# Optimization experiments

Hardware: AMD Instinct MI355X
Metric: run time of the kernel (lower is better)

The kernel has to match this reference:

```python
import jax, jax.numpy as jnp
import numpy as np

HIDDEN = 256
N_PROT = 12288
N_MOL = 6144
N_BATCH = 32


def setup_inputs() -> dict:
    key = jax.random.key(0)
    ks = jax.random.split(key, 10)
    s = 1.0 / np.sqrt(HIDDEN)  # torch Linear default init scale
    inp = {
        "prot_embed": jax.random.normal(ks[0], (N_PROT, HIDDEN), jnp.float32),
        "mol_embed": jax.random.normal(ks[1], (N_MOL, HIDDEN), jnp.float32),
        "prot_batch": jnp.sort(jax.random.randint(ks[2], (N_PROT,), 0, N_BATCH)),
        "mol_batch": jnp.sort(jax.random.randint(ks[3], (N_MOL,), 0, N_BATCH)),
        "Wq": jax.random.uniform(ks[4], (HIDDEN, HIDDEN), jnp.float32, -s, s),
        "bq": jax.random.uniform(ks[5], (HIDDEN,), jnp.float32, -s, s),
        "Wk": jax.random.uniform(ks[6], (HIDDEN, HIDDEN), jnp.float32, -s, s),
        "bk": jax.random.uniform(ks[7], (HIDDEN,), jnp.float32, -s, s),
        "Wv": jax.random.uniform(ks[8], (HIDDEN, HIDDEN), jnp.float32, -s, s),
        "bv": jax.random.uniform(ks[9], (HIDDEN,), jnp.float32, -s, s),
    }
    return inp


def reference(prot_embed, mol_embed, prot_batch, mol_batch, Wq, bq, Wk, bk, Wv, bv):
    # Linear projections (torch nn.Linear: x @ W.T + b)
    Q = prot_embed @ Wq.T + bq            # [N, H]
    K = mol_embed @ Wk.T + bk             # [M, H]
    V = mol_embed @ Wv.T + bv             # [M, H]

    scale = 1.0 / jnp.sqrt(jnp.asarray(Q.shape[-1], Q.dtype))
    scores = (Q @ K.T) * scale            # [N, M]

    # block mask: same-batch pairs only
    mask = prot_batch[:, None] == mol_batch[None, :]   # [N, M] bool
    neg_inf = jnp.asarray(-jnp.inf, scores.dtype)
    scores = jnp.where(mask, scores, neg_inf)

    # stable masked softmax; rows with no valid key -> all zeros
    # (matches torch softmax(-inf row) -> nan -> nan_to_num(0.0))
    row_any = mask.any(axis=-1, keepdims=True)
    mx = jnp.max(scores, axis=-1, keepdims=True)
    mx = jnp.where(row_any, mx, 0.0)
    e = jnp.exp(scores - mx)              # exp(-inf)=0 on masked entries
    denom = jnp.sum(e, axis=-1, keepdims=True)
    attn = e / jnp.where(row_any, denom, 1.0)  # [N, M]

    out = attn @ V                        # [N, H]
    return out, attn
```

## Files before the change

kernel.cpp:

```cpp
#include <hip/hip_runtime.h>

#define NPROT 12288
#define NMOL  6144
#define HID   256
#define NB    32

#define PROT_O 0
#define MOL_O  3145728
#define WQ_O   4718592
#define WK_O   4784128
#define WV_O   4849664
#define BQ_O   4915200
#define BK_O   4915456
#define BV_O   4915712
#define Q_O    4915968
#define K_O    8061696
#define VT_O   9634560
#define END_O  11207424

#define FROWS_BLK 49152

typedef __attribute__((ext_vector_type(4))) float f32x4;
typedef __attribute__((ext_vector_type(8))) short bf16x8;
typedef unsigned short u16;
typedef unsigned int   u32;

__device__ __forceinline__ float b2f(u16 u){
  union { u32 i; float f; } v; v.i = ((u32)u) << 16; return v.f;
}
__device__ __forceinline__ u16 f2b(float f){
  union { float fl; u32 i; } v; v.fl = f;
  u32 i = v.i;
  return (u16)((i + 0x7FFFu + ((i >> 16) & 1u)) >> 16);
}

__device__ __forceinline__ void fill_rows8(float* attnf, int fid){
  float* dst = attnf + (size_t)fid * FROWS_BLK + threadIdx.x * 4;
  f32x4 z = {0.f, 0.f, 0.f, 0.f};
  #pragma unroll 4
  for (int i = 0; i < 48; i++)
    __builtin_nontemporal_store(z, (f32x4*)(dst + i * 1024));
}

__global__ __launch_bounds__(256) void convert_kernel(
    const float* __restrict__ prot, const float* __restrict__ mol,
    const float* __restrict__ Wq, const float* __restrict__ Wk,
    const float* __restrict__ Wv, const float* __restrict__ bq,
    const float* __restrict__ bk, const float* __restrict__ bv,
    const int* __restrict__ pb, const int* __restrict__ mb,
    int* __restrict__ rg, u16* __restrict__ cvt, float* __restrict__ dout)
{
  if (blockIdx.x >= 4801){
    fill_rows8(dout + (size_t)NPROT * HID, blockIdx.x - 4801);
    return;
  }
  int g = blockIdx.x * 256 + threadIdx.x;
  const float* src = nullptr; u16* dst = nullptr; int off = 0;
  if      (g < 786432)  { src = prot; dst = cvt + PROT_O; off = g; }
  else if (g < 1179648) { src = mol;  dst = cvt + MOL_O;  off = g - 786432; }
  else if (g < 1196032) { src = Wq;   dst = cvt + WQ_O;   off = g - 1179648; }
  else if (g < 1212416) { src = Wk;   dst = cvt + WK_O;   off = g - 1196032; }
  else if (g < 1228800) { src = Wv;   dst = cvt + WV_O;   off = g - 1212416; }
  else if (g < 1228864) { src = bq;   dst = cvt + BQ_O;   off = g - 1228800; }
  else if (g < 1228928) { src = bk;   dst = cvt + BK_O;   off = g - 1228864; }
  else if (g < 1228992) { src = bv;   dst = cvt + BV_O;   off = g - 1228928; }
  if (src){
    f32x4 v = *(const f32x4*)(src + (size_t)off * 4);
    ushort4 o;
    o.x = f2b(v[0]); o.y = f2b(v[1]); o.z = f2b(v[2]); o.w = f2b(v[3]);
    *(ushort4*)(dst + (size_t)off * 4) = o;
  }

  if (blockIdx.x == 0 && threadIdx.x < 64){
    int t = threadIdx.x;
    const int* arr = (t < 32) ? pb : mb;
    int n          = (t < 32) ? NPROT : NMOL;
    int target     = (t & 31) + 1;
    int lo = 0, hi = n;
    while (lo < hi){
      int mid = (lo + hi) >> 1;
      if (arr[mid] < target) lo = mid + 1; else hi = mid;
    }
    int end = lo;
    int prev = __shfl(end, t - 1);
    int start = ((t & 31) == 0) ? 0 : prev;
    int b = t & 31;
    if (t < 32){ rg[b] = start; rg[32 + b] = end; }
    else       { rg[64 + b] = start; rg[96 + b] = end; }
  }
}

__global__ __launch_bounds__(256) void proj_kernel(
    const u16* __restrict__ cvt,
    u16* __restrict__ Q, u16* __restrict__ K, u16* __restrict__ Vt,
    float* __restrict__ dout)
{
  __shared__ u16 tlds[4][64][18];
  if (blockIdx.x >= 1536){
    fill_rows8(dout + (size_t)NPROT * HID, blockIdx.x - 1536 + 512);
    return;
  }
  int rowblk = blockIdx.x >> 2, colblk = blockIdx.x & 3;
  int proj;
  if      (rowblk < 192){ proj = 0; }
  else if (rowblk < 288){ proj = 1; rowblk -= 192; }
  else                  { proj = 2; rowblk -= 288; }
  const u16 *X, *W, *B;
  if (proj == 0){ X = cvt + PROT_O; W = cvt + WQ_O; B = cvt + BQ_O; }
  else if (proj == 1){ X = cvt + MOL_O; W = cvt + WK_O; B = cvt + BK_O; }
  else { X = cvt + MOL_O; W = cvt + WV_O; B = cvt + BV_O; }

  int wave = threadIdx.x >> 6, lane = threadIdx.x & 63;
  int m = lane & 15, q = lane >> 4;
  int rowbase = rowblk * 64 + wave * 16;
  int colbase = colblk * 64;

  const u16* arow = X + (size_t)(rowbase + m) * HID;
  f32x4 acc[4] = {};
  for (int k0 = 0; k0 < HID; k0 += 32){
    bf16x8 a = *(const bf16x8*)(arow + k0 + q*8);
    #pragma unroll
    for (int ct = 0; ct < 4; ct++){
      bf16x8 b = *(const bf16x8*)(W + (size_t)(colbase + ct*16 + m) * HID + k0 + q*8);
      acc[ct] = __builtin_amdgcn_mfma_f32_16x16x32_bf16(a, b, acc[ct], 0, 0, 0);
    }
  }

  if (proj < 2){
    u16* O = (proj == 0) ? Q : K;
    #pragma unroll
    for (int ct = 0; ct < 4; ct++){
      int col = colbase + ct*16 + m;
      float bb = b2f(B[col]);
      #pragma unroll
      for (int r = 0; r < 4; r++){
        int row = rowbase + q*4 + r;
        O[(size_t)row * HID + col] = f2b(acc[ct][r] + bb);
      }
    }
  } else {
    #pragma unroll
    for (int ct = 0; ct < 4; ct++){
      int lc = ct*16 + m;
      float bb = b2f(B[colbase + lc]);
      #pragma unroll
      for (int r = 0; r < 4; r++)
        tlds[wave][lc][q*4 + r] = f2b(acc[ct][r] + bb);
    }
    __syncthreads();
    int col = colbase + lane;
    u32 packed[8];
    #pragma unroll
    for (int i = 0; i < 8; i++){
      u16 lo = tlds[wave][lane][2*i];
      u16 hi = tlds[wave][lane][2*i+1];
      packed[i] = (u32)lo | ((u32)hi << 16);
    }
    u16* dst = Vt + (size_t)col * NMOL + rowbase;
    uint4 v0 = {packed[0], packed[1], packed[2], packed[3]};
    uint4 v1 = {packed[4], packed[5], packed[6], packed[7]};
    *(uint4*)dst = v0;
    *(uint4*)(dst + 8) = v1;
  }
}

__global__ __launch_bounds__(256) void attn_kernel(
    const int* __restrict__ rg, const int* __restrict__ pb,
    const u16* __restrict__ Q, const u16* __restrict__ K,
    const u16* __restrict__ Vt, float* __restrict__ dout)
{
  __shared__ u16 P[16][392];
  __shared__ float mxw[4][16];
  __shared__ float smw[4][16];
  const float scale = 0.0625f;
  float* outf  = dout;
  float* attnf = dout + (size_t)NPROT * HID;

  if (blockIdx.x >= 32){
    int fid = (blockIdx.x - 32) + 8 * blockIdx.y;
    int r0 = 8192 + fid * 16;
    f32x4 z = {0.f, 0.f, 0.f, 0.f};
    for (int rr = 0; rr < 16; rr++){
      int row = r0 + rr;
      int bb = pb[row];
      int ms = rg[64 + bb], me = rg[96 + bb];
      float* rowp = attnf + (size_t)row * NMOL;
      int mv = ms & ~3;
      for (int c = threadIdx.x * 4; c < mv; c += 1024)
        __builtin_nontemporal_store(z, (f32x4*)(rowp + c));
      for (int c = mv + threadIdx.x; c < ms; c += 256)
        rowp[c] = 0.f;
      int mu = (me + 3) & ~3;
      for (int c = me + threadIdx.x; c < mu && c < NMOL; c += 256)
        rowp[c] = 0.f;
      for (int c = mu + threadIdx.x * 4; c < NMOL; c += 1024)
        __builtin_nontemporal_store(z, (f32x4*)(rowp + c));
    }
    return;
  }

  int b = blockIdx.y;
  int ps = rg[b], pe = rg[32+b], ms = rg[64+b], me = rg[96+b];
  int Np = pe - ps, Nm = me - ms;
  if (Np <= 0) return;

  int wave = threadIdx.x >> 6, lane = threadIdx.x & 63;
  int m = lane & 15, q = lane >> 4;
  int ntiles = (Np + 15) >> 4;

  int bs = 0, ce = 0;
  if (Nm > 0){ bs = ms & ~31; ce = bs + ((me - bs + 31) & ~31); }

  for (int tile = blockIdx.x; tile < ntiles; tile += 32){
    int row0 = ps + tile * 16;
    int qr = min(row0 + m, NPROT - 1);
    const u16* qrow = Q + (size_t)qr * HID;
    bf16x8 qf[8];
    #pragma unroll
    for (int kk = 0; kk < 8; kk++)
      qf[kk] = *(const bf16x8*)(qrow + kk*32 + q*8);

    if (Nm > 0){
      int myj0 = bs + wave * 16;
      f32x4 sreg[6];
      float mx[4] = {-1e30f, -1e30f, -1e30f, -1e30f};
      #pragma unroll
      for (int c = 0; c < 6; c++){
        int j0 = myj0 + 64*c;
        if (j0 < ce){
          int col = j0 + m;
          bool valid = (col >= ms) && (col < me);
          const u16* krow = K + (size_t)col * HID;
          f32x4 s0 = {0.f,0.f,0.f,0.f}, s1 = {0.f,0.f,0.f,0.f};
          #pragma unroll
          for (int kk = 0; kk < 4; kk++){
            bf16x8 kb0 = *(const bf16x8*)(krow + kk*32 + q*8);
            bf16x8 kb1 = *(const bf16x8*)(krow + (kk+4)*32 + q*8);
            s0 = __builtin_amdgcn_mfma_f32_16x16x32_bf16(qf[kk],   kb0, s0, 0, 0, 0);
            s1 = __builtin_amdgcn_mfma_f32_16x16x32_bf16(qf[kk+4], kb1, s1, 0, 0, 0);
          }
          f32x4 sv;
          #pragma unroll
          for (int r = 0; r < 4; r++)
            sv[r] = valid ? (s0[r] + s1[r]) * scale : -1e30f;
          sreg[c] = sv;
          float cm[4];
          #pragma unroll
          for (int r = 0; r < 4; r++) cm[r] = sv[r];
          #pragma unroll
          for (int d = 1; d < 16; d <<= 1)
            #pragma unroll
            for (int r = 0; r < 4; r++)
              cm[r] = fmaxf(cm[r], __shfl_xor(cm[r], d, 16));
          #pragma unroll
          for (int r = 0; r < 4; r++) mx[r] = fmaxf(mx[r], cm[r]);
        }
      }
      if (m == 0){
        #pragma unroll
        for (int r = 0; r < 4; r++) mxw[wave][q*4 + r] = mx[r];
      }
      __syncthreads();
      float gmx[4];
      #pragma unroll
      for (int r = 0; r < 4; r++){
        int row = q*4 + r;
        float M = mxw[0][row];
        #pragma unroll
        for (int w = 1; w < 4; w++) M = fmaxf(M, mxw[w][row]);
        gmx[r] = M;
      }

      float sm[4] = {0.f, 0.f, 0.f, 0.f};
      #pragma unroll
      for (int c = 0; c < 6; c++){
        int j0 = myj0 + 64*c;
        if (j0 < ce){
          f32x4 e;
          #pragma unroll
          for (int r = 0; r < 4; r++) e[r] = __expf(sreg[c][r] - gmx[r]);
          sreg[c] = e;
          float t[4];
          #pragma unroll
          for (int r = 0; r < 4; r++) t[r] = e[r];
          #pragma unroll
          for (int d = 1; d < 16; d <<= 1)
            #pragma unroll
            for (int r = 0; r < 4; r++)
              t[r] += __shfl_xor(t[r], d, 16);
          #pragma unroll
          for (int r = 0; r < 4; r++) sm[r] += t[r];
        }
      }
      if (m == 0){
        #pragma unroll
        for (int r = 0; r < 4; r++) smw[wave][q*4 + r] = sm[r];
      }
      __syncthreads();
      float ginv[4];
      #pragma unroll
      for (int r = 0; r < 4; r++){
        int row = q*4 + r;
        float S = smw[0][row] + smw[1][row] + smw[2][row] + smw[3][row];
        ginv[r] = (S > 0.f) ? (1.f / S) : 0.f;
      }

      #pragma unroll
      for (int c = 0; c < 6; c++){
        int j0 = myj0 + 64*c;
        if (j0 < ce){
          int col = j0 + m;
          int jl = j0 - bs;
          bool valid = (col >= ms) && (col < me);
          #pragma unroll
          for (int r = 0; r < 4; r++){
            float p = sreg[c][r] * ginv[r];
            P[q*4 + r][jl + m] = f2b(p);
            int row = row0 + q*4 + r;
            if (valid && row < pe)
              __builtin_nontemporal_store(p, attnf + (size_t)row * NMOL + col);
          }
        }
      }
      __syncthreads();

      f32x4 oacc[4] = {};
      for (int j0 = bs; j0 < ce; j0 += 32){
        int jl = j0 - bs;
        bf16x8 a = *(const bf16x8*)(&P[m][jl + q*8]);
        #pragma unroll
        for (int c2 = 0; c2 < 4; c2++){
          int ct = wave*4 + c2;
          bf16x8 vb = *(const bf16x8*)(Vt + (size_t)(ct*16 + m) * NMOL + j0 + q*8);
          oacc[c2] = __builtin_amdgcn_mfma_f32_16x16x32_bf16(a, vb, oacc[c2], 0, 0, 0);
        }
      }
      #pragma unroll
      for (int c2 = 0; c2 < 4; c2++){
        int col = (wave*4 + c2)*16 + m;
        #pragma unroll
        for (int r = 0; r < 4; r++){
          int row = row0 + q*4 + r;
          if (row < pe) outf[(size_t)row * HID + col] = oacc[c2][r];
        }
      }
    } else {
      #pragma unroll
      for (int c2 = 0; c2 < 4; c2++){
        int col = (wave*4 + c2)*16 + m;
        #pragma unroll
        for (int r = 0; r < 4; r++){
          int row = row0 + q*4 + r;
          if (row < pe) outf[(size_t)row * HID + col] = 0.f;
        }
      }
    }
    __syncthreads();
  }
}

extern "C" void kernel_launch(void* const* d_in, const int* in_sizes, int n_in,
                              void* d_out, int out_size, void* d_ws, size_t ws_size,
                              hipStream_t stream)
{
  (void)in_sizes; (void)n_in; (void)out_size;
  const float* prot = (const float*)d_in[0];
  const float* mol  = (const float*)d_in[1];
  const int* pb     = (const int*)d_in[2];
  const int* mb     = (const int*)d_in[3];
  const float* Wq   = (const float*)d_in[4];
  const float* bq   = (const float*)d_in[5];
  const float* Wk   = (const float*)d_in[6];
  const float* bk   = (const float*)d_in[7];
  const float* Wv   = (const float*)d_in[8];
  const float* bv   = (const float*)d_in[9];

  const size_t need = 1024 + (size_t)END_O * 2;
  if (ws_size < need) return;

  char* ws = (char*)d_ws;
  int* rg  = (int*)ws;
  u16* cvt = (u16*)(ws + 1024);
  u16* Qp  = cvt + Q_O;
  u16* Kp  = cvt + K_O;
  u16* Vtp = cvt + VT_O;
  float* out = (float*)d_out;

  convert_kernel<<<dim3(4801 + 512), dim3(256), 0, stream>>>(
      prot, mol, Wq, Wk, Wv, bq, bk, bv, pb, mb, rg, cvt, out);
  proj_kernel<<<dim3(1536 + 512), dim3(256), 0, stream>>>(
      cvt, Qp, Kp, Vtp, out);
  attn_kernel<<<dim3(40, NB), dim3(256), 0, stream>>>(rg, pb, Qp, Kp, Vtp, out);
}
```

Measured before the change: 390.1 us.

## Fuse prot fp32-to-bf16 conversion into Q projection and widen Q/K tiles

The separate bf16 conversion of prot_embed is removed. The Q projection now reads fp32 prot rows directly with nontemporal loads and converts them in registers, so the intermediate bf16 copy is never written or re-read. Q and K blocks now compute all 256 output columns per block (16 accumulator tiles) instead of 64, which cuts redundant A-row reads across column blocks but raises register pressure. The zero-fill block counts are rebalanced between the convert and projection kernels to match the new grid sizes.

```diff
diff --git a/kernel.cpp b/kernel.cpp
--- a/kernel.cpp
+++ b/kernel.cpp
@@ -5,7 +5,6 @@
 #define HID   256
 #define NB    32
 
-#define PROT_O 0
 #define MOL_O  3145728
 #define WQ_O   4718592
 #define WK_O   4784128
@@ -19,6 +18,10 @@
 #define END_O  11207424
 
 #define FROWS_BLK 49152
+#define CVT_BLKS  1729
+#define CVT_FILL  640
+#define PROJ_BLKS 672
+#define PROJ_FILL 384
 
 typedef __attribute__((ext_vector_type(4))) float f32x4;
 typedef __attribute__((ext_vector_type(8))) short bf16x8;
@@ -43,27 +46,26 @@
 }
 
 __global__ __launch_bounds__(256) void convert_kernel(
-    const float* __restrict__ prot, const float* __restrict__ mol,
+    const float* __restrict__ mol,
     const float* __restrict__ Wq, const float* __restrict__ Wk,
     const float* __restrict__ Wv, const float* __restrict__ bq,
     const float* __restrict__ bk, const float* __restrict__ bv,
     const int* __restrict__ pb, const int* __restrict__ mb,
     int* __restrict__ rg, u16* __restrict__ cvt, float* __restrict__ dout)
 {
-  if (blockIdx.x >= 4801){
-    fill_rows8(dout + (size_t)NPROT * HID, blockIdx.x - 4801);
+  if (blockIdx.x >= CVT_BLKS){
+    fill_rows8(dout + (size_t)NPROT * HID, blockIdx.x - CVT_BLKS);
     return;
   }
   int g = blockIdx.x * 256 + threadIdx.x;
   const float* src = nullptr; u16* dst = nullptr; int off = 0;
-  if      (g < 786432)  { src = prot; dst = cvt + PROT_O; off = g; }
-  else if (g < 1179648) { src = mol;  dst = cvt + MOL_O;  off = g - 786432; }
-  else if (g < 1196032) { src = Wq;   dst = cvt + WQ_O;   off = g - 1179648; }
-  else if (g < 1212416) { src = Wk;   dst = cvt + WK_O;   off = g - 1196032; }
-  else if (g < 1228800) { src = Wv;   dst = cvt + WV_O;   off = g - 1212416; }
-  else if (g < 1228864) { src = bq;   dst = cvt + BQ_O;   off = g - 1228800; }
-  else if (g < 1228928) { src = bk;   dst = cvt + BK_O;   off = g - 1228864; }
-  else if (g < 1228992) { src = bv;   dst = cvt + BV_O;   off = g - 1228928; }
+  if      (g < 393216) { src = mol; dst = cvt + MOL_O; off = g; }
+  else if (g < 409600) { src = Wq;  dst = cvt + WQ_O;  off = g - 393216; }
+  else if (g < 425984) { src = Wk;  dst = cvt + WK_O;  off = g - 409600; }
+  else if (g < 442368) { src = Wv;  dst = cvt + WV_O;  off = g - 425984; }
+  else if (g < 442432) { src = bq;  dst = cvt + BQ_O;  off = g - 442368; }
+  else if (g < 442496) { src = bk;  dst = cvt + BK_O;  off = g - 442432; }
+  else if (g < 442560) { src = bv;  dst = cvt + BV_O;  off = g - 442496; }
   if (src){
     f32x4 v = *(const f32x4*)(src + (size_t)off * 4);
     ushort4 o;
@@ -91,27 +93,64 @@
 }
 
 __global__ __launch_bounds__(256) void proj_kernel(
-    const u16* __restrict__ cvt,
+    const float* __restrict__ prot, const u16* __restrict__ cvt,
     u16* __restrict__ Q, u16* __restrict__ K, u16* __restrict__ Vt,
     float* __restrict__ dout)
 {
   __shared__ u16 tlds[4][64][18];
-  if (blockIdx.x >= 1536){
-    fill_rows8(dout + (size_t)NPROT * HID, blockIdx.x - 1536 + 512);
+  int x = blockIdx.x;
+  if (x >= PROJ_BLKS){
+    fill_rows8(dout + (size_t)NPROT * HID, (x - PROJ_BLKS) + CVT_FILL);
     return;
   }
-  int rowblk = blockIdx.x >> 2, colblk = blockIdx.x & 3;
-  int proj;
-  if      (rowblk < 192){ proj = 0; }
-  else if (rowblk < 288){ proj = 1; rowblk -= 192; }
-  else                  { proj = 2; rowblk -= 288; }
-  const u16 *X, *W, *B;
-  if (proj == 0){ X = cvt + PROT_O; W = cvt + WQ_O; B = cvt + BQ_O; }
-  else if (proj == 1){ X = cvt + MOL_O; W = cvt + WK_O; B = cvt + BK_O; }
-  else { X = cvt + MOL_O; W = cvt + WV_O; B = cvt + BV_O; }
-
   int wave = threadIdx.x >> 6, lane = threadIdx.x & 63;
   int m = lane & 15, q = lane >> 4;
+
+  if (x < 288){
+    bool isQ = (x < 192);
+    int rowbase = (isQ ? x : (x - 192)) * 64 + wave * 16;
+    const u16* W = cvt + (isQ ? WQ_O : WK_O);
+    const u16* B = cvt + (isQ ? BQ_O : BK_O);
+    u16* O = isQ ? Q : K;
+
+    f32x4 acc[16] = {};
+    for (int k0 = 0; k0 < HID; k0 += 32){
+      bf16x8 a;
+      if (isQ){
+        const float* ar = prot + (size_t)(rowbase + m) * HID + k0 + q*8;
+        f32x4 v0 = __builtin_nontemporal_load((const f32x4*)ar);
+        f32x4 v1 = __builtin_nontemporal_load((const f32x4*)(ar + 4));
+        a[0]=(short)f2b(v0[0]); a[1]=(short)f2b(v0[1]);
+        a[2]=(short)f2b(v0[2]); a[3]=(short)f2b(v0[3]);
+        a[4]=(short)f2b(v1[0]); a[5]=(short)f2b(v1[1]);
+        a[6]=(short)f2b(v1[2]); a[7]=(short)f2b(v1[3]);
+      } else {
+        a = *(const bf16x8*)(cvt + MOL_O + (size_t)(rowbase + m) * HID + k0 + q*8);
+      }
+      #pragma unroll
+      for (int ct = 0; ct < 16; ct++){
+        bf16x8 b = *(const bf16x8*)(W + (size_t)(ct*16 + m) * HID + k0 + q*8);
+        acc[ct] = __builtin_amdgcn_mfma_f32_16x16x32_bf16(a, b, acc[ct], 0, 0, 0);
+      }
+    }
+    #pragma unroll
+    for (int ct = 0; ct < 16; ct++){
+      int col = ct*16 + m;
+      float bb = b2f(B[col]);
+      #pragma unroll
+      for (int r = 0; r < 4; r++){
+        int row = rowbase + q*4 + r;
+        O[(size_t)row * HID + col] = f2b(acc[ct][r] + bb);
+      }
+    }
+    return;
+  }
+
+  int v = x - 288;
+  int rowblk = v >> 2, colblk = v & 3;
+  const u16* X = cvt + MOL_O;
+  const u16* W = cvt + WV_O;
+  const u16* B = cvt + BV_O;
   int rowbase = rowblk * 64 + wave * 16;
   int colbase = colblk * 64;
 
@@ -125,43 +164,28 @@
       acc[ct] = __builtin_amdgcn_mfma_f32_16x16x32_bf16(a, b, acc[ct], 0, 0, 0);
     }
   }
-
-  if (proj < 2){
-    u16* O = (proj == 0) ? Q : K;
+  #pragma unroll
+  for (int ct = 0; ct < 4; ct++){
+    int lc = ct*16 + m;
+    float bb = b2f(B[colbase + lc]);
     #pragma unroll
-    for (int ct = 0; ct < 4; ct++){
-      int col = colbase + ct*16 + m;
-      float bb = b2f(B[col]);
-      #pragma unroll
-      for (int r = 0; r < 4; r++){
-        int row = rowbase + q*4 + r;
-        O[(size_t)row * HID + col] = f2b(acc[ct][r] + bb);
-      }
-    }
-  } else {
-    #pragma unroll
-    for (int ct = 0; ct < 4; ct++){
-      int lc = ct*16 + m;
-      float bb = b2f(B[colbase + lc]);
-      #pragma unroll
-      for (int r = 0; r < 4; r++)
-        tlds[wave][lc][q*4 + r] = f2b(acc[ct][r] + bb);
-    }
-    __syncthreads();
-    int col = colbase + lane;
-    u32 packed[8];
-    #pragma unroll
-    for (int i = 0; i < 8; i++){
-      u16 lo = tlds[wave][lane][2*i];
-      u16 hi = tlds[wave][lane][2*i+1];
-      packed[i] = (u32)lo | ((u32)hi << 16);
-    }
-    u16* dst = Vt + (size_t)col * NMOL + rowbase;
-    uint4 v0 = {packed[0], packed[1], packed[2], packed[3]};
-    uint4 v1 = {packed[4], packed[5], packed[6], packed[7]};
-    *(uint4*)dst = v0;
-    *(uint4*)(dst + 8) = v1;
-  }
+    for (int r = 0; r < 4; r++)
+      tlds[wave][lc][q*4 + r] = f2b(acc[ct][r] + bb);
+  }
+  __syncthreads();
+  int col = colbase + lane;
+  u32 packed[8];
+  #pragma unroll
+  for (int i = 0; i < 8; i++){
+    u16 lo = tlds[wave][lane][2*i];
+    u16 hi = tlds[wave][lane][2*i+1];
+    packed[i] = (u32)lo | ((u32)hi << 16);
+  }
+  u16* dst = Vt + (size_t)col * NMOL + rowbase;
+  uint4 v0 = {packed[0], packed[1], packed[2], packed[3]};
+  uint4 v1 = {packed[4], packed[5], packed[6], packed[7]};
+  *(uint4*)dst = v0;
+  *(uint4*)(dst + 8) = v1;
 }
 
 __global__ __launch_bounds__(256) void attn_kernel(
@@ -386,9 +410,9 @@
   u16* Vtp = cvt + VT_O;
   float* out = (float*)d_out;
 
-  convert_kernel<<<dim3(4801 + 512), dim3(256), 0, stream>>>(
-      prot, mol, Wq, Wk, Wv, bq, bk, bv, pb, mb, rg, cvt, out);
-  proj_kernel<<<dim3(1536 + 512), dim3(256), 0, stream>>>(
-      cvt, Qp, Kp, Vtp, out);
+  convert_kernel<<<dim3(CVT_BLKS + CVT_FILL), dim3(256), 0, stream>>>(
+      mol, Wq, Wk, Wv, bq, bk, bv, pb, mb, rg, cvt, out);
+  proj_kernel<<<dim3(PROJ_BLKS + PROJ_FILL), dim3(256), 0, stream>>>(
+      prot, cvt, Qp, Kp, Vtp, out);
   attn_kernel<<<dim3(40, NB), dim3(256), 0, stream>>>(rg, pb, Qp, Kp, Vtp, out);
 }
```

New measurement: 394.0 us. No clear change (+1.0%).
